# Optimization experiments

Hardware: AMD Instinct MI355X
Metric: run time of the kernel (lower is better)

The kernel has to match this reference:

```python
import jax, jax.numpy as jnp
import numpy as np

D_MODEL = 1024
NUM_HEADS = 16
HEAD_DIM = D_MODEL // NUM_HEADS


def setup_inputs() -> dict:
    key = jax.random.key(0)
    k1, k2, k3, k4, k5 = jax.random.split(key, 5)
    B, S = 2, 2048
    X = jax.random.normal(k1, (B, S, D_MODEL), dtype=jnp.float32)
    Wqkv = jax.random.normal(k2, (3 * D_MODEL, D_MODEL), dtype=jnp.float32) * 0.02
    bqkv = jax.random.normal(k3, (3 * D_MODEL,), dtype=jnp.float32) * 0.02
    Wo = jax.random.normal(k4, (D_MODEL, D_MODEL), dtype=jnp.float32) * 0.02
    bo = jax.random.normal(k5, (D_MODEL,), dtype=jnp.float32) * 0.02
    return {"X": X, "Wqkv": Wqkv, "bqkv": bqkv, "Wo": Wo, "bo": bo}


def reference(X, Wqkv, bqkv, Wo, bo):
    B, S, D = X.shape
    # fused QKV projection (torch Linear: x @ W.T + b)
    qkv = X @ Wqkv.T + bqkv                                  # [B, S, 3D]
    qkv = qkv.reshape(B, S, NUM_HEADS, 3 * HEAD_DIM)
    qkv = jnp.transpose(qkv, (0, 2, 1, 3))                   # [B, H, S, 3*hd]
    q, k, v = jnp.split(qkv, 3, axis=-1)                     # each [B, H, S, hd]
    # naive scaled dot-product attention (materializes full SxS scores)
    scale = 1.0 / jnp.sqrt(jnp.asarray(HEAD_DIM, dtype=X.dtype))
    scores = jnp.einsum("bhqd,bhkd->bhqk", q, k) * scale     # [B, H, S, S]
    attn = jax.nn.softmax(scores, axis=-1)
    values = jnp.einsum("bhqk,bhkd->bhqd", attn, v)          # [B, H, S, hd]
    values = jnp.transpose(values, (0, 2, 1, 3)).reshape(B, S, D)
    return values @ Wo.T + bo
```

## Files before the change

### kernel.cpp

```cpp
#include <hip/hip_runtime.h>

#define DM    1024
#define NH    16
#define HD    64
#define SEQ   2048
#define BATCH 2
#define NQKV  3072
#define MTOT  4096

using half2v = __attribute__((ext_vector_type(2))) _Float16;
using half4  = __attribute__((ext_vector_type(4))) _Float16;
using half8  = __attribute__((ext_vector_type(8))) _Float16;
using f32x4  = __attribute__((ext_vector_type(4))) float;

typedef const __attribute__((address_space(1))) unsigned int* gp_t;
typedef __attribute__((address_space(3))) unsigned int* lp_t;

__device__ __forceinline__ void gl2lds16(const void* g, void* l) {
    __builtin_amdgcn_global_load_lds((gp_t)g, (lp_t)l, 16, 0, 0);
}

__device__ __forceinline__ f32x4 fzero4() {
    f32x4 v; v[0] = 0.f; v[1] = 0.f; v[2] = 0.f; v[3] = 0.f; return v;
}

__device__ __forceinline__ int sw8(int row, int col) {
    return (row << 6) | ((((col >> 3) ^ row) & 7) << 3) | (col & 7);
}

#define CSCALE 0.18033688011112042f

__device__ __forceinline__ half2v expp2(float a, float b) {
    return __builtin_bit_cast(half2v, __builtin_amdgcn_cvt_pkrtz(
        __builtin_amdgcn_exp2f(a), __builtin_amdgcn_exp2f(b)));
}

__global__ __launch_bounds__(256) void cvt_all(const float* __restrict__ X,
                                               const float* __restrict__ W1,
                                               const float* __restrict__ W2,
                                               const float* __restrict__ bqkv,
                                               float* __restrict__ bscaled,
                                               _Float16* __restrict__ out) {
    const int nX = MTOT * DM / 4, nW1 = NQKV * DM / 4, nW2 = DM * DM / 4;
    int i = blockIdx.x * 256 + threadIdx.x;
    if (i < NQKV) {
        const float b = bqkv[i];
        bscaled[i] = ((i % 192) < 64) ? b * CSCALE : b;
    }
    if (i >= nX + nW1 + nW2) return;
    float4 f;
    float sc = 1.0f;
    if (i < nX) {
        f = reinterpret_cast<const float4*>(X)[i];
    } else if (i < nX + nW1) {
        const int off = i - nX;
        f = reinterpret_cast<const float4*>(W1)[off];
        const int row = off >> 8;
        if ((row % 192) < 64) sc = CSCALE;
    } else {
        f = reinterpret_cast<const float4*>(W2)[i - nX - nW1];
    }
    half4 h;
    h[0] = (_Float16)(f.x * sc); h[1] = (_Float16)(f.y * sc);
    h[2] = (_Float16)(f.z * sc); h[3] = (_Float16)(f.w * sc);
    reinterpret_cast<half4*>(out)[i] = h;
}

template <bool OUT_F16>
__global__ __launch_bounds__(256) void gemm_nt(const _Float16* __restrict__ A,
                                               const _Float16* __restrict__ B,
                                               const float* __restrict__ bias,
                                               void* __restrict__ Cout,
                                               int M, int N, int K) {
    __shared__ _Float16 lA[128 * 64];
    __shared__ _Float16 lB[128 * 64];
    const int tid = threadIdx.x;
    const int m0 = blockIdx.y * 128, n0 = blockIdx.x * 128;
    const int wave = tid >> 6, lane = tid & 63, quad = lane >> 4, l15 = lane & 15;
    const int wm = (wave & 1) * 64, wn = (wave >> 1) * 64;

    f32x4 acc[4][4];
#pragma unroll
    for (int i = 0; i < 4; ++i)
#pragma unroll
        for (int j = 0; j < 4; ++j) acc[i][j] = fzero4();

    const int cperm = (((tid & 7) ^ (tid >> 3)) & 7) * 8;
    const _Float16* Ab = A + (long)(m0 + (tid >> 3)) * K + cperm;
    const _Float16* Bb = B + (long)(n0 + (tid >> 3)) * K + cperm;
    char* lAp = (char*)lA + tid * 16;
    char* lBp = (char*)lB + tid * 16;

    for (int kt = 0; kt < K; kt += 64) {
        __syncthreads();
#pragma unroll
        for (int j = 0; j < 4; ++j) {
            gl2lds16(Ab + (long)j * 32 * K + kt, lAp + j * 4096);
            gl2lds16(Bb + (long)j * 32 * K + kt, lBp + j * 4096);
        }
        __syncthreads();
#pragma unroll
        for (int ks = 0; ks < 2; ++ks) {
            half8 af[4], bfr[4];
#pragma unroll
            for (int t = 0; t < 4; ++t) {
                af[t]  = *(const half8*)(lA + sw8(wm + t * 16 + l15, ks * 32 + quad * 8));
                bfr[t] = *(const half8*)(lB + sw8(wn + t * 16 + l15, ks * 32 + quad * 8));
            }
#pragma unroll
            for (int mt = 0; mt < 4; ++mt)
#pragma unroll
                for (int nt = 0; nt < 4; ++nt)
                    acc[mt][nt] = __builtin_amdgcn_mfma_f32_16x16x32_f16(
                        af[mt], bfr[nt], acc[mt][nt], 0, 0, 0);
        }
    }

    float bs[4];
#pragma unroll
    for (int nt = 0; nt < 4; ++nt) bs[nt] = bias[n0 + wn + nt * 16 + l15];

#pragma unroll
    for (int mt = 0; mt < 4; ++mt) {
#pragma unroll
        for (int r = 0; r < 4; ++r) {
            const int m = m0 + wm + mt * 16 + quad * 4 + r;
#pragma unroll
            for (int nt = 0; nt < 4; ++nt) {
                const int n = n0 + wn + nt * 16 + l15;
                const float v = acc[mt][nt][r] + bs[nt];
                if constexpr (OUT_F16)
                    ((_Float16*)Cout)[(long)m * N + n] = (_Float16)v;
                else
                    ((float*)Cout)[(long)m * N + n] = v;
            }
        }
    }
}

template <bool OUT_F16>
__global__ __launch_bounds__(256) void gemm_nt_64(const _Float16* __restrict__ A,
                                                  const _Float16* __restrict__ B,
                                                  const float* __restrict__ bias,
                                                  void* __restrict__ Cout,
                                                  int M, int N, int K) {
    __shared__ _Float16 lA[64 * 64];
    __shared__ _Float16 lB[128 * 64];
    const int tid = threadIdx.x;
    const int m0 = blockIdx.y * 64, n0 = blockIdx.x * 128;
    const int wave = tid >> 6, lane = tid & 63, quad = lane >> 4, l15 = lane & 15;
    const int wm = (wave & 1) * 32, wn = (wave >> 1) * 64;

    f32x4 acc[2][4];
#pragma unroll
    for (int i = 0; i < 2; ++i)
#pragma unroll
        for (int j = 0; j < 4; ++j) acc[i][j] = fzero4();

    const int cperm = (((tid & 7) ^ (tid >> 3)) & 7) * 8;
    const _Float16* Ab = A + (long)(m0 + (tid >> 3)) * K + cperm;
    const _Float16* Bb = B + (long)(n0 + (tid >> 3)) * K + cperm;
    char* lAp = (char*)lA + tid * 16;
    char* lBp = (char*)lB + tid * 16;

    for (int kt = 0; kt < K; kt += 64) {
        __syncthreads();
#pragma unroll
        for (int j = 0; j < 2; ++j)
            gl2lds16(Ab + (long)j * 32 * K + kt, lAp + j * 4096);
#pragma unroll
        for (int j = 0; j < 4; ++j)
            gl2lds16(Bb + (long)j * 32 * K + kt, lBp + j * 4096);
        __syncthreads();
#pragma unroll
        for (int ks = 0; ks < 2; ++ks) {
            half8 af[2], bfr[4];
#pragma unroll
            for (int t = 0; t < 2; ++t)
                af[t] = *(const half8*)(lA + sw8(wm + t * 16 + l15, ks * 32 + quad * 8));
#pragma unroll
            for (int t = 0; t < 4; ++t)
                bfr[t] = *(const half8*)(lB + sw8(wn + t * 16 + l15, ks * 32 + quad * 8));
#pragma unroll
            for (int mt = 0; mt < 2; ++mt)
#pragma unroll
                for (int nt = 0; nt < 4; ++nt)
                    acc[mt][nt] = __builtin_amdgcn_mfma_f32_16x16x32_f16(
                        af[mt], bfr[nt], acc[mt][nt], 0, 0, 0);
        }
    }

    float bs[4];
#pragma unroll
    for (int nt = 0; nt < 4; ++nt) bs[nt] = bias[n0 + wn + nt * 16 + l15];

#pragma unroll
    for (int mt = 0; mt < 2; ++mt) {
#pragma unroll
        for (int r = 0; r < 4; ++r) {
            const int m = m0 + wm + mt * 16 + quad * 4 + r;
#pragma unroll
            for (int nt = 0; nt < 4; ++nt) {
                const int n = n0 + wn + nt * 16 + l15;
                const float v = acc[mt][nt][r] + bs[nt];
                if constexpr (OUT_F16)
                    ((_Float16*)Cout)[(long)m * N + n] = (_Float16)v;
                else
                    ((float*)Cout)[(long)m * N + n] = v;
            }
        }
    }
}

__global__ __launch_bounds__(256) void repack_v(const _Float16* __restrict__ qkvh,
                                                _Float16* __restrict__ vt) {
    const int b = blockIdx.z, h = blockIdx.y, s0 = blockIdx.x * 32;
    const int d = threadIdx.x & 63, si = threadIdx.x >> 6;
    const _Float16* src = qkvh + (long)(b * SEQ + s0 + si * 8) * NQKV + h * 192 + 128 + d;
    half8 v;
#pragma unroll
    for (int i = 0; i < 8; ++i) v[i] = src[(long)i * NQKV];
    *(half8*)(vt + (long)((b * NH + h) * HD + d) * SEQ + s0 + si * 8) = v;
}

__global__ __launch_bounds__(256) void attn_flash(const _Float16* __restrict__ qkv,
                                                  const _Float16* __restrict__ vt,
                                                  _Float16* __restrict__ aout) {
    __shared__ _Float16 lQ[128 * 64];
    __shared__ _Float16 lK[2][64 * 64];
    __shared__ _Float16 lV[2][64 * 64];

    const int L = blockIdx.x + 16 * blockIdx.y + 256 * blockIdx.z;
    const int c = L & 7, j = L >> 3;
    const int pair = c * 4 + (j >> 4);
    const int b = pair >> 4, h = pair & 15;
    const int q0 = (j & 15) * 128;

    const int tid = threadIdx.x;
    const int wave = tid >> 6, lane = tid & 63, quad = lane >> 4, l15 = lane & 15;
    const int cperm8 = (((tid & 7) ^ (tid >> 3)) & 7) * 8;

    const _Float16* qsrc = qkv + (long)(b * SEQ + q0 + (tid >> 3)) * NQKV + h * 192 + cperm8;
#pragma unroll
    for (int jq = 0; jq < 4; ++jq)
        gl2lds16(qsrc + (long)jq * 32 * NQKV, (char*)lQ + jq * 4096 + tid * 16);

    const _Float16* ksrc = qkv + (long)(b * SEQ + (tid >> 3)) * NQKV + h * 192 + 64 + cperm8;
    const _Float16* vsrc = vt + (long)((b * NH + h) * HD + (tid >> 3)) * SEQ + cperm8;

#pragma unroll
    for (int jj = 0; jj < 2; ++jj) {
        gl2lds16(ksrc + (long)(jj * 32) * NQKV, (char*)lK[0] + jj * 4096 + tid * 16);
        gl2lds16(vsrc + (long)(jj * 32) * SEQ,  (char*)lV[0] + jj * 4096 + tid * 16);
    }
    __syncthreads();

    half8 qf[2][2];
#pragma unroll
    for (int qt = 0; qt < 2; ++qt)
#pragma unroll
        for (int ks = 0; ks < 2; ++ks)
            qf[qt][ks] = *(const half8*)(lQ + sw8(wave * 32 + qt * 16 + l15, ks * 32 + quad * 8));

    f32x4 O[2][4];
#pragma unroll
    for (int qt = 0; qt < 2; ++qt)
#pragma unroll
        for (int dt = 0; dt < 4; ++dt) O[qt][dt] = fzero4();
    f32x4 lsum[2] = {fzero4(), fzero4()};

    half8 ones;
#pragma unroll
    for (int i = 0; i < 8; ++i) ones[i] = (_Float16)1.0f;

    for (int it = 0; it < 32; ++it) {
        const int cur = it & 1;
        if (it < 31) {
            const int s0n = (it + 1) * 64;
#pragma unroll
            for (int jj = 0; jj < 2; ++jj) {
                gl2lds16(ksrc + (long)(s0n + jj * 32) * NQKV, (char*)lK[cur ^ 1] + jj * 4096 + tid * 16);
                gl2lds16(vsrc + (long)(jj * 32) * SEQ + s0n,  (char*)lV[cur ^ 1] + jj * 4096 + tid * 16);
            }
        }

#pragma unroll
        for (int t = 0; t < 2; ++t) {
            f32x4 s[2][2];
            s[0][0] = fzero4(); s[0][1] = fzero4();
            s[1][0] = fzero4(); s[1][1] = fzero4();
#pragma unroll
            for (int tt = 0; tt < 2; ++tt) {
#pragma unroll
                for (int ks = 0; ks < 2; ++ks) {
                    half8 kf = *(const half8*)(lK[cur] + sw8((2 * t + tt) * 16 + l15, ks * 32 + quad * 8));
                    s[0][tt] = __builtin_amdgcn_mfma_f32_16x16x32_f16(kf, qf[0][ks], s[0][tt], 0, 0, 0);
                    s[1][tt] = __builtin_amdgcn_mfma_f32_16x16x32_f16(kf, qf[1][ks], s[1][tt], 0, 0, 0);
                }
            }
            half8 pf[2];
#pragma unroll
            for (int qt = 0; qt < 2; ++qt) {
                half2v p01 = expp2(s[qt][0][0], s[qt][0][1]);
                half2v p23 = expp2(s[qt][0][2], s[qt][0][3]);
                half2v p45 = expp2(s[qt][1][0], s[qt][1][1]);
                half2v p67 = expp2(s[qt][1][2], s[qt][1][3]);
                half4 lo = __builtin_shufflevector(p01, p23, 0, 1, 2, 3);
                half4 hi = __builtin_shufflevector(p45, p67, 0, 1, 2, 3);
                pf[qt] = __builtin_shufflevector(lo, hi, 0, 1, 2, 3, 4, 5, 6, 7);
                lsum[qt] = __builtin_amdgcn_mfma_f32_16x16x32_f16(pf[qt], ones, lsum[qt], 0, 0, 0);
            }
#pragma unroll
            for (int dt = 0; dt < 4; ++dt) {
                const int vrow = dt * 16 + l15;
                half4 v0 = *(const half4*)(lV[cur] + sw8(vrow, t * 32 + quad * 4));
                half4 v1 = *(const half4*)(lV[cur] + sw8(vrow, t * 32 + quad * 4 + 16));
                half8 vf = __builtin_shufflevector(v0, v1, 0, 1, 2, 3, 4, 5, 6, 7);
                O[0][dt] = __builtin_amdgcn_mfma_f32_16x16x32_f16(pf[0], vf, O[0][dt], 0, 0, 0);
                O[1][dt] = __builtin_amdgcn_mfma_f32_16x16x32_f16(pf[1], vf, O[1][dt], 0, 0, 0);
            }
        }
        __syncthreads();
    }

#pragma unroll
    for (int qt = 0; qt < 2; ++qt) {
#pragma unroll
        for (int r = 0; r < 4; ++r) {
            const float lr = 1.0f / lsum[qt][r];
            const int row = b * SEQ + q0 + wave * 32 + qt * 16 + quad * 4 + r;
#pragma unroll
            for (int dt = 0; dt < 4; ++dt)
                aout[(long)row * DM + h * HD + dt * 16 + l15] =
                    (_Float16)(O[qt][dt][r] * lr);
        }
    }
}

extern "C" void kernel_launch(void* const* d_in, const int* in_sizes, int n_in,
                              void* d_out, int out_size, void* d_ws, size_t ws_size,
                              hipStream_t stream) {
    const float* X    = (const float*)d_in[0];
    const float* Wqkv = (const float*)d_in[1];
    const float* bqkv = (const float*)d_in[2];
    const float* Wo   = (const float*)d_in[3];
    const float* bo   = (const float*)d_in[4];

    char* ws = (char*)d_ws;
    _Float16* Xh   = (_Float16*)(ws);
    _Float16* Wqh  = (_Float16*)(ws + (size_t)8  * 1048576);
    _Float16* Woh  = (_Float16*)(ws + (size_t)14 * 1048576);
    _Float16* qkvh = (_Float16*)(ws + (size_t)16 * 1048576);
    _Float16* vth  = (_Float16*)(ws + (size_t)40 * 1048576);
    _Float16* atth = (_Float16*)(ws + (size_t)48 * 1048576);
    float* bscaled = (float*)(ws + (size_t)48 * 1048576);

    const int ncvt = (MTOT * DM + NQKV * DM + DM * DM) / 4;
    cvt_all<<<(ncvt + 255) / 256, 256, 0, stream>>>(X, Wqkv, Wo, bqkv, bscaled, Xh);

    gemm_nt<true><<<dim3(NQKV / 128, MTOT / 128), 256, 0, stream>>>(
        Xh, Wqh, bscaled, qkvh, MTOT, NQKV, DM);

    repack_v<<<dim3(SEQ / 32, NH, BATCH), 256, 0, stream>>>(qkvh, vth);

    attn_flash<<<dim3(SEQ / 128, NH, BATCH), 256, 0, stream>>>(qkvh, vth, atth);

    gemm_nt_64<false><<<dim3(DM / 128, MTOT / 64), 256, 0, stream>>>(
        atth, Woh, bo, d_out, MTOT, DM, DM);
}
```

Before: 196.1 us.

## Alias Q staging buffer with K/V LDS and permute V repack for half8 reads

```diff
diff --git a/kernel.cpp b/kernel.cpp
--- a/kernel.cpp
+++ b/kernel.cpp
@@ -216,19 +216,20 @@
                                                 _Float16* __restrict__ vt) {
     const int b = blockIdx.z, h = blockIdx.y, s0 = blockIdx.x * 32;
     const int d = threadIdx.x & 63, si = threadIdx.x >> 6;
-    const _Float16* src = qkvh + (long)(b * SEQ + s0 + si * 8) * NQKV + h * 192 + 128 + d;
+    const _Float16* src = qkvh + (long)(b * SEQ + s0) * NQKV + h * 192 + 128 + d;
     half8 v;
 #pragma unroll
-    for (int i = 0; i < 8; ++i) v[i] = src[(long)i * NQKV];
+    for (int hi = 0; hi < 2; ++hi)
+#pragma unroll
+        for (int r = 0; r < 4; ++r)
+            v[hi * 4 + r] = src[(long)(hi * 16 + si * 4 + r) * NQKV];
     *(half8*)(vt + (long)((b * NH + h) * HD + d) * SEQ + s0 + si * 8) = v;
 }
 
 __global__ __launch_bounds__(256) void attn_flash(const _Float16* __restrict__ qkv,
                                                   const _Float16* __restrict__ vt,
                                                   _Float16* __restrict__ aout) {
-    __shared__ _Float16 lQ[128 * 64];
-    __shared__ _Float16 lK[2][64 * 64];
-    __shared__ _Float16 lV[2][64 * 64];
+    __shared__ _Float16 lKV[4][64 * 64];
 
     const int L = blockIdx.x + 16 * blockIdx.y + 256 * blockIdx.z;
     const int c = L & 7, j = L >> 3;
@@ -243,35 +244,37 @@
     const _Float16* qsrc = qkv + (long)(b * SEQ + q0 + (tid >> 3)) * NQKV + h * 192 + cperm8;
 #pragma unroll
     for (int jq = 0; jq < 4; ++jq)
-        gl2lds16(qsrc + (long)jq * 32 * NQKV, (char*)lQ + jq * 4096 + tid * 16);
+        gl2lds16(qsrc + (long)jq * 32 * NQKV, (char*)lKV + jq * 4096 + tid * 16);
+    __syncthreads();
+
+    half8 qf[2][2];
+#pragma unroll
+    for (int qt = 0; qt < 2; ++qt)
+#pragma unroll
+        for (int ks = 0; ks < 2; ++ks)
+            qf[qt][ks] = *(const half8*)(lKV[0] + sw8(wave * 32 + qt * 16 + l15, ks * 32 + quad * 8));
+    __syncthreads();
+
+    f32x4 O[2][4];
+#pragma unroll
+    for (int qt = 0; qt < 2; ++qt)
+#pragma unroll
+        for (int dt = 0; dt < 4; ++dt) O[qt][dt] = fzero4();
+    f32x4 lsum[2] = {fzero4(), fzero4()};
+
+    half8 ones;
+#pragma unroll
+    for (int i = 0; i < 8; ++i) ones[i] = (_Float16)1.0f;
 
     const _Float16* ksrc = qkv + (long)(b * SEQ + (tid >> 3)) * NQKV + h * 192 + 64 + cperm8;
     const _Float16* vsrc = vt + (long)((b * NH + h) * HD + (tid >> 3)) * SEQ + cperm8;
 
 #pragma unroll
     for (int jj = 0; jj < 2; ++jj) {
-        gl2lds16(ksrc + (long)(jj * 32) * NQKV, (char*)lK[0] + jj * 4096 + tid * 16);
-        gl2lds16(vsrc + (long)(jj * 32) * SEQ,  (char*)lV[0] + jj * 4096 + tid * 16);
+        gl2lds16(ksrc + (long)(jj * 32) * NQKV, (char*)lKV[0] + jj * 4096 + tid * 16);
+        gl2lds16(vsrc + (long)(jj * 32) * SEQ,  (char*)lKV[2] + jj * 4096 + tid * 16);
     }
     __syncthreads();
-
-    half8 qf[2][2];
-#pragma unroll
-    for (int qt = 0; qt < 2; ++qt)
-#pragma unroll
-        for (int ks = 0; ks < 2; ++ks)
-            qf[qt][ks] = *(const half8*)(lQ + sw8(wave * 32 + qt * 16 + l15, ks * 32 + quad * 8));
-
-    f32x4 O[2][4];
-#pragma unroll
-    for (int qt = 0; qt < 2; ++qt)
-#pragma unroll
-        for (int dt = 0; dt < 4; ++dt) O[qt][dt] = fzero4();
-    f32x4 lsum[2] = {fzero4(), fzero4()};
-
-    half8 ones;
-#pragma unroll
-    for (int i = 0; i < 8; ++i) ones[i] = (_Float16)1.0f;
 
     for (int it = 0; it < 32; ++it) {
         const int cur = it & 1;
@@ -279,10 +282,12 @@
             const int s0n = (it + 1) * 64;
 #pragma unroll
             for (int jj = 0; jj < 2; ++jj) {
-                gl2lds16(ksrc + (long)(s0n + jj * 32) * NQKV, (char*)lK[cur ^ 1] + jj * 4096 + tid * 16);
-                gl2lds16(vsrc + (long)(jj * 32) * SEQ + s0n,  (char*)lV[cur ^ 1] + jj * 4096 + tid * 16);
-            }
-        }
+                gl2lds16(ksrc + (long)(s0n + jj * 32) * NQKV, (char*)lKV[cur ^ 1] + jj * 4096 + tid * 16);
+                gl2lds16(vsrc + (long)(jj * 32) * SEQ + s0n,  (char*)lKV[2 + (cur ^ 1)] + jj * 4096 + tid * 16);
+            }
+        }
+        const _Float16* lK = lKV[cur];
+        const _Float16* lV = lKV[2 + cur];
 
 #pragma unroll
         for (int t = 0; t < 2; ++t) {
@@ -293,7 +298,7 @@
             for (int tt = 0; tt < 2; ++tt) {
 #pragma unroll
                 for (int ks = 0; ks < 2; ++ks) {
-                    half8 kf = *(const half8*)(lK[cur] + sw8((2 * t + tt) * 16 + l15, ks * 32 + quad * 8));
+                    half8 kf = *(const half8*)(lK + sw8((2 * t + tt) * 16 + l15, ks * 32 + quad * 8));
                     s[0][tt] = __builtin_amdgcn_mfma_f32_16x16x32_f16(kf, qf[0][ks], s[0][tt], 0, 0, 0);
                     s[1][tt] = __builtin_amdgcn_mfma_f32_16x16x32_f16(kf, qf[1][ks], s[1][tt], 0, 0, 0);
                 }
@@ -312,10 +317,7 @@
             }
 #pragma unroll
             for (int dt = 0; dt < 4; ++dt) {
-                const int vrow = dt * 16 + l15;
-                half4 v0 = *(const half4*)(lV[cur] + sw8(vrow, t * 32 + quad * 4));
-                half4 v1 = *(const half4*)(lV[cur] + sw8(vrow, t * 32 + quad * 4 + 16));
-                half8 vf = __builtin_shufflevector(v0, v1, 0, 1, 2, 3, 4, 5, 6, 7);
+                half8 vf = *(const half8*)(lV + sw8(dt * 16 + l15, t * 32 + quad * 8));
                 O[0][dt] = __builtin_amdgcn_mfma_f32_16x16x32_f16(pf[0], vf, O[0][dt], 0, 0, 0);
                 O[1][dt] = __builtin_amdgcn_mfma_f32_16x16x32_f16(pf[1], vf, O[1][dt], 0, 0, 0);
             }
```

After: 184.7 us. 1.06x faster.
